# Optimization experiments

Measured on AMD Instinct MI355X. Metric: run time of the kernel, lower is better.

Reference implementation:

```python
import jax, jax.numpy as jnp
import numpy as np

TAU = 0.1
EPS = 1e-8


def setup_inputs() -> dict:
    key = jax.random.key(0)
    k1, k2, k3 = jax.random.split(key, 3)
    B, D = 4096, 256
    features = jax.random.normal(k1, (B, D), dtype=jnp.float32)
    pos_features = jax.random.normal(k2, (B, D), dtype=jnp.float32)
    labels = jax.random.randint(k3, (B,), 0, 64, dtype=jnp.int64)
    return {"features": features, "pos_features": pos_features, "labels": labels}


def reference(features, pos_features, labels):
    # concat image and positive features / duplicate labels
    f = jnp.concatenate([features, pos_features], axis=0)          # [N, D], N = 2B
    lab = jnp.concatenate([labels, labels], axis=0)                # [N]
    N = f.shape[0]

    # cosine similarity: mm(a, a.T) / clamp(w * w.T, 1e-8)
    w = jnp.linalg.norm(f, axis=1, keepdims=True)                  # [N, 1]
    logits = (f @ f.T) / jnp.clip(w * w.T, EPS)                    # [N, N]
    z = logits / TAU

    diag = jnp.eye(N, dtype=bool)
    neg_inf = jnp.asarray(-jnp.inf, dtype=z.dtype)

    # denominator: logsumexp over all off-diagonal entries per row
    loss_all = jnp.sum(jax.nn.logsumexp(jnp.where(diag, neg_inf, z), axis=1))

    # positives: for each row, logsumexp over same-label off-diagonal entries.
    # This vectorizes the original python loop over unique labels: the union of
    # the per-label sub-matrices (diagonal removed) is exactly this mask.
    same = (lab[:, None] == lab[None, :]) & ~diag                  # [N, N]
    loss_pos = jnp.sum(jax.nn.logsumexp(jnp.where(same, z, neg_inf), axis=1))

    return loss_all - loss_pos
```

## Files before the change

### kernel.cpp

```cpp
#include <hip/hip_runtime.h>
#include <hip/hip_bf16.h>
#include <stdint.h>

#define NROWS 8192
#define DDIM  256
#define BM    128
#define BN    128
#define BK    64
#define KSTEPS (DDIM / BK)
#define NTILE (NROWS / BM)
#define NTRI  (NTILE * (NTILE + 1) / 2)
#define SCEXP 14.4269504088896340736f

#define COL_STRIDE2 5
#define ROW_STRIDE2 18
#define ROWAP_OFF   5120
#define SMEM_BYTES  65536

typedef __attribute__((ext_vector_type(8))) short short8;
typedef __attribute__((ext_vector_type(4))) float f32x4;

typedef const __attribute__((address_space(1))) uint32_t glb_u32;
typedef __attribute__((address_space(3))) uint32_t lds_u32;

__device__ __forceinline__ void load_lds16(const unsigned short* g, unsigned short* l) {
  __builtin_amdgcn_global_load_lds((glb_u32*)g, (lds_u32*)l, 16, 0, 0);
}

__device__ __forceinline__ unsigned short f2bf(float x) {
  __hip_bfloat16 h = __float2bfloat16(x);
  return *reinterpret_cast<unsigned short*>(&h);
}

__global__ void __launch_bounds__(256)
milnce_prep(const float* __restrict__ feat, const float* __restrict__ pos,
            const int* __restrict__ labels, unsigned short* __restrict__ fb,
            int* __restrict__ lab, float* __restrict__ S_all,
            float* __restrict__ S_pos, float* __restrict__ out) {
  const int wave = threadIdx.x >> 6;
  const int lane = threadIdx.x & 63;
  const int row  = blockIdx.x * 4 + wave;

  const float* src = (row < 4096) ? (feat + (size_t)row * DDIM)
                                  : (pos + (size_t)(row - 4096) * DDIM);
  float4 v = ((const float4*)src)[lane];

  float ss = v.x*v.x + v.y*v.y + v.z*v.z + v.w*v.w;
  #pragma unroll
  for (int m = 1; m < 64; m <<= 1) ss += __shfl_xor(ss, m, 64);
  const float inv = 1.0f / sqrtf(ss);

  ushort4 o;
  o.x = f2bf(v.x * inv); o.y = f2bf(v.y * inv);
  o.z = f2bf(v.z * inv); o.w = f2bf(v.w * inv);
  ((ushort4*)(fb + (size_t)row * DDIM))[lane] = o;

  const int tid = blockIdx.x * 256 + threadIdx.x;
  if (tid < NROWS) {
    lab[tid]   = labels[tid & 4095];
    S_all[tid] = 0.0f;
    S_pos[tid] = 0.0f;
  }
  if (tid == 0) out[0] = 0.0f;
}

__global__ void __launch_bounds__(256, 2)
milnce_gemm(const unsigned short* __restrict__ fb, const int* __restrict__ lab,
            float* __restrict__ S_all, float* __restrict__ S_pos) {
  __shared__ __align__(16) char smem[SMEM_BYTES];

  int t = blockIdx.x;
  int d = (int)((129.0f - sqrtf(16641.0f - 8.0f * (float)t)) * 0.5f);
  while (d * (129 - d) / 2 > t) --d;
  while ((d + 1) * (128 - d) / 2 <= t) ++d;
  const int rem = t - d * (129 - d) / 2;
  const int bi = rem, bj = rem + d;

  const int tid  = threadIdx.x;
  const int wave = tid >> 6;
  const int lane = tid & 63;
  const int quad = lane >> 4;
  const int l15  = lane & 15;
  const int wm   = wave >> 1;
  const int wn   = wave & 1;
  const int rowBase = bi * BM;
  const int colBase = bj * BN;

  f32x4 acc[4][4];
  #pragma unroll
  for (int i = 0; i < 4; ++i)
    #pragma unroll
    for (int j = 0; j < 4; ++j) acc[i][j] = (f32x4){0.f, 0.f, 0.f, 0.f};

  const unsigned short* gA[4];
  const unsigned short* gB[4];
  #pragma unroll
  for (int i = 0; i < 4; ++i) {
    const int s = i * 256 + wave * 64 + lane;
    const int r = s >> 3;
    const int g = (s & 7) ^ (r & 7);
    gA[i] = fb + (size_t)(rowBase + r) * DDIM + g * 8;
    gB[i] = fb + (size_t)(colBase + r) * DDIM + g * 8;
  }
  unsigned short* lds = (unsigned short*)smem;
  const int dstW = wave * 512;

  #pragma unroll
  for (int i = 0; i < 4; ++i) load_lds16(gA[i], lds + dstW + i * 2048);
  #pragma unroll
  for (int i = 0; i < 4; ++i) load_lds16(gB[i], lds + 8192 + dstW + i * 2048);

  const int jx   = (quad ^ (l15 & 7)) * 8;
  const int rowA = (wm * 64 + l15) * BK;
  const int rowB = (wn * 64 + l15) * BK;

  #pragma unroll
  for (int kt = 0; kt < KSTEPS; ++kt) {
    const int cur = kt & 1;
    if (kt + 1 < KSTEPS) {
      const int nxtOff = (cur ^ 1) * 16384;
      const int ko = (kt + 1) * BK;
      #pragma unroll
      for (int i = 0; i < 4; ++i)
        load_lds16(gA[i] + ko, lds + nxtOff + dstW + i * 2048);
      #pragma unroll
      for (int i = 0; i < 4; ++i)
        load_lds16(gB[i] + ko, lds + nxtOff + 8192 + dstW + i * 2048);
      asm volatile("s_waitcnt vmcnt(8)" ::: "memory");
    } else {
      asm volatile("s_waitcnt vmcnt(0)" ::: "memory");
    }
    __builtin_amdgcn_s_barrier();

    const unsigned short* As = lds + cur * 16384;
    const unsigned short* Bs = As + 8192;
    #pragma unroll
    for (int kk = 0; kk < 2; ++kk) {
      short8 a[4], b[4];
      const int jo = jx ^ (kk * 32);
      #pragma unroll
      for (int mi = 0; mi < 4; ++mi)
        a[mi] = *(const short8*)&As[rowA + mi * 1024 + jo];
      #pragma unroll
      for (int ni = 0; ni < 4; ++ni)
        b[ni] = *(const short8*)&Bs[rowB + ni * 1024 + jo];
      __builtin_amdgcn_s_setprio(1);
      #pragma unroll
      for (int mi = 0; mi < 4; ++mi)
        #pragma unroll
        for (int ni = 0; ni < 4; ++ni)
          acc[mi][ni] = __builtin_amdgcn_mfma_f32_16x16x32_bf16(a[mi], b[ni], acc[mi][ni], 0, 0, 0);
      __builtin_amdgcn_s_setprio(0);
    }
    asm volatile("s_waitcnt lgkmcnt(0)" ::: "memory");
    __builtin_amdgcn_s_barrier();
  }

  float2* colAP = (float2*)smem;
  float2* rowAP = (float2*)(smem + ROWAP_OFF);

  int cl[4], colg[4];
  #pragma unroll
  for (int ni = 0; ni < 4; ++ni) {
    colg[ni] = colBase + wn * 64 + ni * 16 + l15;
    cl[ni]   = lab[colg[ni]];
  }

  const bool offdiag = (bi != bj);
  float2 capk[4] = {{0.f,0.f},{0.f,0.f},{0.f,0.f},{0.f,0.f}};

  if (offdiag) {
    #pragma unroll
    for (int mi = 0; mi < 4; ++mi) {
      const int rbase = wm * 64 + mi * 16 + quad * 4;
      const int4 rl4 = *(const int4*)&lab[rowBase + rbase];
      #pragma unroll
      for (int r = 0; r < 4; ++r) {
        const int rl = (r == 0) ? rl4.x : (r == 1) ? rl4.y : (r == 2) ? rl4.z : rl4.w;
        float sx = 0.f, sy = 0.f;
        #pragma unroll
        for (int ni = 0; ni < 4; ++ni) {
          float e  = exp2f(__builtin_fmaf(acc[mi][ni][r], SCEXP, -SCEXP));
          float ep = (rl == cl[ni]) ? e : 0.f;
          capk[ni].x += e; capk[ni].y += ep;
          sx += e; sy += ep;
        }
        rowAP[(rbase + r) * ROW_STRIDE2 + wn * 16 + l15] = make_float2(sx, sy);
      }
    }
  } else {
    #pragma unroll
    for (int mi = 0; mi < 4; ++mi) {
      const int rbase = wm * 64 + mi * 16 + quad * 4;
      const int4 rl4 = *(const int4*)&lab[rowBase + rbase];
      #pragma unroll
      for (int r = 0; r < 4; ++r) {
        const int rl = (r == 0) ? rl4.x : (r == 1) ? rl4.y : (r == 2) ? rl4.z : rl4.w;
        const int rowg = rowBase + rbase + r;
        #pragma unroll
        for (int ni = 0; ni < 4; ++ni) {
          float e = exp2f(__builtin_fmaf(acc[mi][ni][r], SCEXP, -SCEXP));
          if (rowg == colg[ni]) e = 0.f;
          float ep = (rl == cl[ni]) ? e : 0.f;
          capk[ni].x += e; capk[ni].y += ep;
        }
      }
    }
  }

  #pragma unroll
  for (int ni = 0; ni < 4; ++ni)
    colAP[(wn * 64 + ni * 16 + l15) * COL_STRIDE2 + quad] = capk[ni];

  __syncthreads();

  if (tid < 128) {
    const float2* cp = &colAP[tid * COL_STRIDE2];
    float2 c0 = cp[0], c1 = cp[1], c2 = cp[2], c3 = cp[3];
    atomicAdd(&S_all[colBase + tid], (c0.x + c1.x) + (c2.x + c3.x));
    atomicAdd(&S_pos[colBase + tid], (c0.y + c1.y) + (c2.y + c3.y));
  } else if (offdiag) {
    const int rr = tid - 128;
    const float2* rp = &rowAP[rr * ROW_STRIDE2];
    float sx = 0.f, sy = 0.f;
    #pragma unroll
    for (int i = 0; i < 16; ++i) { sx += rp[i].x; sy += rp[i].y; }
    atomicAdd(&S_all[rowBase + rr], sx);
    atomicAdd(&S_pos[rowBase + rr], sy);
  }
}

__global__ void __launch_bounds__(256)
milnce_final(const float* __restrict__ S_all, const float* __restrict__ S_pos,
             float* __restrict__ out) {
  const int i = blockIdx.x * 256 + threadIdx.x;
  float s = logf(S_all[i]) - logf(S_pos[i]);
  #pragma unroll
  for (int m = 1; m < 64; m <<= 1) s += __shfl_xor(s, m, 64);
  __shared__ float red[4];
  if ((threadIdx.x & 63) == 0) red[threadIdx.x >> 6] = s;
  __syncthreads();
  if (threadIdx.x == 0) atomicAdd(out, (red[0] + red[1]) + (red[2] + red[3]));
}

extern "C" void kernel_launch(void* const* d_in, const int* in_sizes, int n_in,
                              void* d_out, int out_size, void* d_ws, size_t ws_size,
                              hipStream_t stream) {
  const float* feat   = (const float*)d_in[0];
  const float* pos    = (const float*)d_in[1];
  const int*   labels = (const int*)d_in[2];

  char* ws = (char*)d_ws;
  unsigned short* fb    = (unsigned short*)ws;
  int*            lab   = (int*)  (ws + 4u * 1024 * 1024);
  float*          S_all = (float*)(ws + 4u * 1024 * 1024 + 32 * 1024);
  float*          S_pos = (float*)(ws + 4u * 1024 * 1024 + 64 * 1024);
  float*          out   = (float*)d_out;

  hipLaunchKernelGGL(milnce_prep, dim3(NROWS / 4), dim3(256), 0, stream,
                     feat, pos, labels, fb, lab, S_all, S_pos, out);
  hipLaunchKernelGGL(milnce_gemm, dim3(NTRI), dim3(256), 0, stream,
                     fb, lab, S_all, S_pos);
  hipLaunchKernelGGL(milnce_final, dim3(32), dim3(256), 0, stream,
                     S_all, S_pos, out);
}
```

Before: 95.74 us.

## Enlarge GEMM tiles to 256x256 with 8 waves and split-phase pipelined loads

Grows the symmetric-tile GEMM from 128x128 to 256x256 blocks with 512 threads and BK=32, which cuts the number of triangle tiles and the redundant global loads per output. The K loop is split into two MFMA phases that interleave the next-stage A and B loads with compute, using sched barriers and priority hints. The epilogue replaces LDS-based column partials with wave shuffles and direct atomics, and merges the diagonal and off-diagonal paths. In exchange, register pressure rises (acc[8][4] across 512 threads) and there are fewer blocks to fill the CUs.

```diff
diff --git a/kernel.cpp b/kernel.cpp
--- a/kernel.cpp
+++ b/kernel.cpp
@@ -4,18 +4,16 @@
 
 #define NROWS 8192
 #define DDIM  256
-#define BM    128
-#define BN    128
-#define BK    64
+#define BM    256
+#define BN    256
+#define BK    32
 #define KSTEPS (DDIM / BK)
 #define NTILE (NROWS / BM)
 #define NTRI  (NTILE * (NTILE + 1) / 2)
 #define SCEXP 14.4269504088896340736f
 
-#define COL_STRIDE2 5
+#define SMEM_BYTES  65536
 #define ROW_STRIDE2 18
-#define ROWAP_OFF   5120
-#define SMEM_BYTES  65536
 
 typedef __attribute__((ext_vector_type(8))) short short8;
 typedef __attribute__((ext_vector_type(4))) float f32x4;
@@ -64,16 +62,17 @@
   if (tid == 0) out[0] = 0.0f;
 }
 
-__global__ void __launch_bounds__(256, 2)
+__global__ void __launch_bounds__(512, 2)
 milnce_gemm(const unsigned short* __restrict__ fb, const int* __restrict__ lab,
             float* __restrict__ S_all, float* __restrict__ S_pos) {
   __shared__ __align__(16) char smem[SMEM_BYTES];
+  unsigned short* lds = (unsigned short*)smem;
 
   int t = blockIdx.x;
-  int d = (int)((129.0f - sqrtf(16641.0f - 8.0f * (float)t)) * 0.5f);
-  while (d * (129 - d) / 2 > t) --d;
-  while ((d + 1) * (128 - d) / 2 <= t) ++d;
-  const int rem = t - d * (129 - d) / 2;
+  int d = (int)((65.0f - sqrtf(4225.0f - 8.0f * (float)t)) * 0.5f);
+  while (d * (65 - d) / 2 > t) --d;
+  while ((d + 1) * (64 - d) / 2 <= t) ++d;
+  const int rem = t - d * (65 - d) / 2;
   const int bi = rem, bj = rem + d;
 
   const int tid  = threadIdx.x;
@@ -81,83 +80,92 @@
   const int lane = tid & 63;
   const int quad = lane >> 4;
   const int l15  = lane & 15;
-  const int wm   = wave >> 1;
-  const int wn   = wave & 1;
+  const int wm   = wave >> 2;
+  const int wn   = wave & 3;
   const int rowBase = bi * BM;
   const int colBase = bj * BN;
 
-  f32x4 acc[4][4];
-  #pragma unroll
-  for (int i = 0; i < 4; ++i)
+  f32x4 acc[8][4];
+  #pragma unroll
+  for (int i = 0; i < 8; ++i)
     #pragma unroll
     for (int j = 0; j < 4; ++j) acc[i][j] = (f32x4){0.f, 0.f, 0.f, 0.f};
 
-  const unsigned short* gA[4];
-  const unsigned short* gB[4];
-  #pragma unroll
-  for (int i = 0; i < 4; ++i) {
-    const int s = i * 256 + wave * 64 + lane;
-    const int r = s >> 3;
-    const int g = (s & 7) ^ (r & 7);
-    gA[i] = fb + (size_t)(rowBase + r) * DDIM + g * 8;
-    gB[i] = fb + (size_t)(colBase + r) * DDIM + g * 8;
-  }
-  unsigned short* lds = (unsigned short*)smem;
-  const int dstW = wave * 512;
-
-  #pragma unroll
-  for (int i = 0; i < 4; ++i) load_lds16(gA[i], lds + dstW + i * 2048);
-  #pragma unroll
-  for (int i = 0; i < 4; ++i) load_lds16(gB[i], lds + 8192 + dstW + i * 2048);
-
-  const int jx   = (quad ^ (l15 & 7)) * 8;
-  const int rowA = (wm * 64 + l15) * BK;
-  const int rowB = (wn * 64 + l15) * BK;
+  const unsigned short *gA0, *gA1, *gB0, *gB1;
+  {
+    const int s0 = tid;
+    const int p0 = s0 >> 3, j0 = (s0 & 7) ^ (p0 & 7);
+    const int r0 = p0 * 2 + (j0 >> 2), o0 = j0 & 3;
+    const int s1 = 512 + tid;
+    const int p1 = s1 >> 3, j1 = (s1 & 7) ^ (p1 & 7);
+    const int r1 = p1 * 2 + (j1 >> 2), o1 = j1 & 3;
+    gA0 = fb + (size_t)(rowBase + r0) * DDIM + o0 * 8;
+    gA1 = fb + (size_t)(rowBase + r1) * DDIM + o1 * 8;
+    gB0 = fb + (size_t)(colBase + r0) * DDIM + o0 * 8;
+    gB1 = fb + (size_t)(colBase + r1) * DDIM + o1 * 8;
+  }
+  const int dst0 = (wave * 64) * 8;
+  const int dst1 = (512 + wave * 64) * 8;
+
+  auto stageA = [&](int kt1, int bufS) {
+    load_lds16(gA0 + kt1 * BK, lds + bufS + dst0);
+    load_lds16(gA1 + kt1 * BK, lds + bufS + dst1);
+  };
+  auto stageB = [&](int kt1, int bufS) {
+    load_lds16(gB0 + kt1 * BK, lds + bufS + 8192 + dst0);
+    load_lds16(gB1 + kt1 * BK, lds + bufS + 8192 + dst1);
+  };
+
+  const int key  = ((l15 & 1) * 4 + quad) ^ ((l15 >> 1) & 7);
+  const int aOff = (wm * 64 + (l15 >> 1)) * 64 + key * 8;
+  const int bOff = 8192 + (wn * 32 + (l15 >> 1)) * 64 + key * 8;
+
+  stageA(0, 0); stageB(0, 0);
+  asm volatile("s_waitcnt vmcnt(0)" ::: "memory");
+  __builtin_amdgcn_s_barrier();
 
   #pragma unroll
   for (int kt = 0; kt < KSTEPS; ++kt) {
-    const int cur = kt & 1;
-    if (kt + 1 < KSTEPS) {
-      const int nxtOff = (cur ^ 1) * 16384;
-      const int ko = (kt + 1) * BK;
-      #pragma unroll
-      for (int i = 0; i < 4; ++i)
-        load_lds16(gA[i] + ko, lds + nxtOff + dstW + i * 2048);
-      #pragma unroll
-      for (int i = 0; i < 4; ++i)
-        load_lds16(gB[i] + ko, lds + nxtOff + 8192 + dstW + i * 2048);
-      asm volatile("s_waitcnt vmcnt(8)" ::: "memory");
-    } else {
-      asm volatile("s_waitcnt vmcnt(0)" ::: "memory");
-    }
-    __builtin_amdgcn_s_barrier();
-
-    const unsigned short* As = lds + cur * 16384;
-    const unsigned short* Bs = As + 8192;
-    #pragma unroll
-    for (int kk = 0; kk < 2; ++kk) {
-      short8 a[4], b[4];
-      const int jo = jx ^ (kk * 32);
-      #pragma unroll
-      for (int mi = 0; mi < 4; ++mi)
-        a[mi] = *(const short8*)&As[rowA + mi * 1024 + jo];
+    const int bufS  = (kt & 1) * 16384;
+    const int nbufS = bufS ^ 16384;
+    const unsigned short* As = lds + bufS;
+
+    short8 a[4], b[4];
+    if (kt + 1 < KSTEPS) stageA(kt + 1, nbufS);
+    #pragma unroll
+    for (int mi = 0; mi < 4; ++mi) a[mi] = *(const short8*)&As[aOff + mi * 512];
+    #pragma unroll
+    for (int ni = 0; ni < 4; ++ni) b[ni] = *(const short8*)&As[bOff + ni * 512];
+    __builtin_amdgcn_s_barrier();
+    asm volatile("s_waitcnt lgkmcnt(0)" ::: "memory");
+    __builtin_amdgcn_sched_barrier(0);
+    __builtin_amdgcn_s_setprio(1);
+    #pragma unroll
+    for (int mi = 0; mi < 4; ++mi)
       #pragma unroll
       for (int ni = 0; ni < 4; ++ni)
-        b[ni] = *(const short8*)&Bs[rowB + ni * 1024 + jo];
-      __builtin_amdgcn_s_setprio(1);
+        acc[mi][ni] = __builtin_amdgcn_mfma_f32_16x16x32_bf16(a[mi], b[ni], acc[mi][ni], 0, 0, 0);
+    __builtin_amdgcn_s_setprio(0);
+    __builtin_amdgcn_s_barrier();
+    if (kt + 1 < KSTEPS) stageB(kt + 1, nbufS);
+    #pragma unroll
+    for (int mi = 0; mi < 4; ++mi) a[mi] = *(const short8*)&As[aOff + (mi + 4) * 512];
+    __builtin_amdgcn_s_barrier();
+    asm volatile("s_waitcnt lgkmcnt(0)" ::: "memory");
+    __builtin_amdgcn_sched_barrier(0);
+    __builtin_amdgcn_s_setprio(1);
+    #pragma unroll
+    for (int mi = 0; mi < 4; ++mi)
       #pragma unroll
-      for (int mi = 0; mi < 4; ++mi)
-        #pragma unroll
-        for (int ni = 0; ni < 4; ++ni)
-          acc[mi][ni] = __builtin_amdgcn_mfma_f32_16x16x32_bf16(a[mi], b[ni], acc[mi][ni], 0, 0, 0);
-      __builtin_amdgcn_s_setprio(0);
-    }
-    asm volatile("s_waitcnt lgkmcnt(0)" ::: "memory");
-    __builtin_amdgcn_s_barrier();
-  }
-
-  float2* colAP = (float2*)smem;
-  float2* rowAP = (float2*)(smem + ROWAP_OFF);
+      for (int ni = 0; ni < 4; ++ni)
+        acc[mi + 4][ni] = __builtin_amdgcn_mfma_f32_16x16x32_bf16(a[mi], b[ni], acc[mi + 4][ni], 0, 0, 0);
+    __builtin_amdgcn_s_setprio(0);
+    if (kt + 1 < KSTEPS) asm volatile("s_waitcnt vmcnt(0)" ::: "memory");
+    __builtin_amdgcn_s_barrier();
+  }
+  __syncthreads();
+
+  float2* rowAP = (float2*)smem;
 
   int cl[4], colg[4];
   #pragma unroll
@@ -169,64 +177,52 @@
   const bool offdiag = (bi != bj);
   float2 capk[4] = {{0.f,0.f},{0.f,0.f},{0.f,0.f},{0.f,0.f}};
 
-  if (offdiag) {
-    #pragma unroll
-    for (int mi = 0; mi < 4; ++mi) {
-      const int rbase = wm * 64 + mi * 16 + quad * 4;
-      const int4 rl4 = *(const int4*)&lab[rowBase + rbase];
+  #pragma unroll
+  for (int mi = 0; mi < 8; ++mi) {
+    const int rbase = wm * 128 + mi * 16 + quad * 4;
+    const int4 rl4 = *(const int4*)&lab[rowBase + rbase];
+    #pragma unroll
+    for (int r = 0; r < 4; ++r) {
+      const int rl = (r == 0) ? rl4.x : (r == 1) ? rl4.y : (r == 2) ? rl4.z : rl4.w;
+      const int rowg = rowBase + rbase + r;
+      float sx = 0.f, sy = 0.f;
       #pragma unroll
-      for (int r = 0; r < 4; ++r) {
-        const int rl = (r == 0) ? rl4.x : (r == 1) ? rl4.y : (r == 2) ? rl4.z : rl4.w;
-        float sx = 0.f, sy = 0.f;
-        #pragma unroll
-        for (int ni = 0; ni < 4; ++ni) {
-          float e  = exp2f(__builtin_fmaf(acc[mi][ni][r], SCEXP, -SCEXP));
-          float ep = (rl == cl[ni]) ? e : 0.f;
-          capk[ni].x += e; capk[ni].y += ep;
-          sx += e; sy += ep;
-        }
-        rowAP[(rbase + r) * ROW_STRIDE2 + wn * 16 + l15] = make_float2(sx, sy);
+      for (int ni = 0; ni < 4; ++ni) {
+        float e = exp2f(__builtin_fmaf(acc[mi][ni][r], SCEXP, -SCEXP));
+        if (!offdiag && rowg == colg[ni]) e = 0.f;
+        float ep = (rl == cl[ni]) ? e : 0.f;
+        capk[ni].x += e; capk[ni].y += ep;
+        sx += e; sy += ep;
+      }
+      if (offdiag) {
+        sx += __shfl_xor(sx, 4, 64); sx += __shfl_xor(sx, 8, 64);
+        sy += __shfl_xor(sy, 4, 64); sy += __shfl_xor(sy, 8, 64);
+        if (l15 < 4)
+          rowAP[(rbase + r) * ROW_STRIDE2 + wn * 4 + l15] = make_float2(sx, sy);
       }
     }
-  } else {
-    #pragma unroll
-    for (int mi = 0; mi < 4; ++mi) {
-      const int rbase = wm * 64 + mi * 16 + quad * 4;
-      const int4 rl4 = *(const int4*)&lab[rowBase + rbase];
-      #pragma unroll
-      for (int r = 0; r < 4; ++r) {
-        const int rl = (r == 0) ? rl4.x : (r == 1) ? rl4.y : (r == 2) ? rl4.z : rl4.w;
-        const int rowg = rowBase + rbase + r;
-        #pragma unroll
-        for (int ni = 0; ni < 4; ++ni) {
-          float e = exp2f(__builtin_fmaf(acc[mi][ni][r], SCEXP, -SCEXP));
-          if (rowg == colg[ni]) e = 0.f;
-          float ep = (rl == cl[ni]) ? e : 0.f;
-          capk[ni].x += e; capk[ni].y += ep;
-        }
-      }
+  }
+
+  #pragma unroll
+  for (int ni = 0; ni < 4; ++ni) {
+    float x = capk[ni].x, y = capk[ni].y;
+    x += __shfl_xor(x, 16, 64); x += __shfl_xor(x, 32, 64);
+    y += __shfl_xor(y, 16, 64); y += __shfl_xor(y, 32, 64);
+    if (quad == 0) {
+      atomicAdd(&S_all[colg[ni]], x);
+      atomicAdd(&S_pos[colg[ni]], y);
     }
   }
 
-  #pragma unroll
-  for (int ni = 0; ni < 4; ++ni)
-    colAP[(wn * 64 + ni * 16 + l15) * COL_STRIDE2 + quad] = capk[ni];
-
   __syncthreads();
 
-  if (tid < 128) {
-    const float2* cp = &colAP[tid * COL_STRIDE2];
-    float2 c0 = cp[0], c1 = cp[1], c2 = cp[2], c3 = cp[3];
-    atomicAdd(&S_all[colBase + tid], (c0.x + c1.x) + (c2.x + c3.x));
-    atomicAdd(&S_pos[colBase + tid], (c0.y + c1.y) + (c2.y + c3.y));
-  } else if (offdiag) {
-    const int rr = tid - 128;
-    const float2* rp = &rowAP[rr * ROW_STRIDE2];
+  if (offdiag && tid < 256) {
+    const float2* rp = rowAP + tid * ROW_STRIDE2;
     float sx = 0.f, sy = 0.f;
     #pragma unroll
     for (int i = 0; i < 16; ++i) { sx += rp[i].x; sy += rp[i].y; }
-    atomicAdd(&S_all[rowBase + rr], sx);
-    atomicAdd(&S_pos[rowBase + rr], sy);
+    atomicAdd(&S_all[rowBase + tid], sx);
+    atomicAdd(&S_pos[rowBase + tid], sy);
   }
 }
 
@@ -259,7 +255,7 @@
 
   hipLaunchKernelGGL(milnce_prep, dim3(NROWS / 4), dim3(256), 0, stream,
                      feat, pos, labels, fb, lab, S_all, S_pos, out);
-  hipLaunchKernelGGL(milnce_gemm, dim3(NTRI), dim3(256), 0, stream,
+  hipLaunchKernelGGL(milnce_gemm, dim3(NTRI), dim3(512), 0, stream,
                      fb, lab, S_all, S_pos);
   hipLaunchKernelGGL(milnce_final, dim3(32), dim3(256), 0, stream,
                      S_all, S_pos, out);
```

Result: slower. 131.8 us (+37.7%).
